# Kernel optimization log

Measured on AMD Instinct MI355X. Metric: run time of the kernel, lower is better.

## Reference

```python
import jax, jax.numpy as jnp
import numpy as np

N = 100000
E = 1600000
IN_C, HID_C, OUT_C = 128, 256, 64
EPS = 1e-5


def _glorot(key, shape):
    fan_in, fan_out = shape
    lim = float(np.sqrt(6.0 / (fan_in + fan_out)))
    return jax.random.uniform(key, shape, jnp.float32, -lim, lim)


def sage_conv(x, src, dst, deg_inv, W_l, b_l, W_r):
    # mean aggregation of neighbor features into target nodes
    msg_sum = jax.ops.segment_sum(x[src], dst, num_segments=N)  # [N, d]
    mean = msg_sum * deg_inv[:, None]
    return mean @ W_l + b_l + x @ W_r


def batch_norm(x, gamma, beta, rm, rv):
    return (x - rm) * jax.lax.rsqrt(rv + EPS) * gamma + beta


def setup_inputs() -> dict:
    key = jax.random.key(0)
    ks = jax.random.split(key, 10)
    x = jax.random.normal(ks[0], (N, IN_C), jnp.float32)
    edge_index = jax.random.randint(ks[1], (2, E), 0, N, jnp.int64)
    inp = {
        "x": x,
        "edge_index": edge_index,
        # layer 1: SAGEConv(IN_C -> HID_C) + BN
        "W1l": _glorot(ks[2], (IN_C, HID_C)),
        "b1l": jnp.zeros((HID_C,), jnp.float32),
        "W1r": _glorot(ks[3], (IN_C, HID_C)),
        "g1": jnp.ones((HID_C,), jnp.float32),
        "be1": jnp.zeros((HID_C,), jnp.float32),
        "rm1": 0.1 * jax.random.normal(ks[4], (HID_C,), jnp.float32),
        "rv1": jnp.ones((HID_C,), jnp.float32),
        # layer 2: SAGEConv(HID_C -> HID_C) + BN
        "W2l": _glorot(ks[5], (HID_C, HID_C)),
        "b2l": jnp.zeros((HID_C,), jnp.float32),
        "W2r": _glorot(ks[6], (HID_C, HID_C)),
        "g2": jnp.ones((HID_C,), jnp.float32),
        "be2": jnp.zeros((HID_C,), jnp.float32),
        "rm2": 0.1 * jax.random.normal(ks[7], (HID_C,), jnp.float32),
        "rv2": jnp.ones((HID_C,), jnp.float32),
        # classifier: SAGEConv(HID_C -> OUT_C)
        "Wcl": _glorot(ks[8], (HID_C, OUT_C)),
        "bcl": jnp.zeros((OUT_C,), jnp.float32),
        "Wcr": _glorot(ks[9], (HID_C, OUT_C)),
    }
    return inp


def reference(x, edge_index, W1l, b1l, W1r, g1, be1, rm1, rv1,
              W2l, b2l, W2r, g2, be2, rm2, rv2, Wcl, bcl, Wcr):
    src, dst = edge_index[0], edge_index[1]
    deg = jax.ops.segment_sum(jnp.ones((E,), jnp.float32), dst, num_segments=N)
    deg_inv = jnp.where(deg > 0, 1.0 / jnp.maximum(deg, 1.0), 0.0)

    h = sage_conv(x, src, dst, deg_inv, W1l, b1l, W1r)
    h = jax.nn.relu(batch_norm(h, g1, be1, rm1, rv1))
    # dropout is identity in eval mode (training=False)
    h = sage_conv(h, src, dst, deg_inv, W2l, b2l, W2r)
    h = jax.nn.relu(batch_norm(h, g2, be2, rm2, rv2))
    return sage_conv(h, src, dst, deg_inv, Wcl, bcl, Wcr)
```

## Files before the change

### kernel.cpp

```cpp
#include <hip/hip_runtime.h>
#include <stdint.h>

#define NN 100000
#define EE 1600000
#define IN_C 128
#define HID_C 256
#define OUT_C 64

#define NB 391
#define CAP 5120
#define K3_NPT 25
#define K3_BLOCKS 250

typedef unsigned short bf16_t;
typedef unsigned int u32;
typedef __attribute__((ext_vector_type(8))) short bf16x8;
typedef __attribute__((ext_vector_type(4))) float f32x4;

__device__ __forceinline__ float b2f(unsigned short u){
  unsigned int x = ((unsigned int)u) << 16;
  return __uint_as_float(x);
}
__device__ __forceinline__ unsigned short f2b(float f){
  unsigned int x = __float_as_uint(f);
  unsigned int r = x + 0x7FFFu + ((x >> 16) & 1u);
  return (unsigned short)(r >> 16);
}

#define GL16(gp, lp) __builtin_amdgcn_global_load_lds( \
    (const __attribute__((address_space(1))) void*)(gp), \
    (__attribute__((address_space(3))) void*)(lp), 16, 0, 0)


__global__ __launch_bounds__(256) void bcount_k(const int* __restrict__ ei,
    int* __restrict__ bcnt){
  __shared__ int h[NB];
  int t = threadIdx.x;
  int o = 0;
  for (int i = t; i < 1024; i += 256) o |= ei[2*i + 1];
  h[t] = o; __syncthreads();
  for (int s = 128; s > 0; s >>= 1){
    if (t < s) h[t] |= h[t + s];
    __syncthreads();
  }
  int i64 = (h[0] == 0) ? 1 : 0;
  __syncthreads();
  for (int i = t; i < NB; i += 256) h[i] = 0;
  __syncthreads();
  int base = blockIdx.x * (256 * K3_NPT);
  #pragma unroll
  for (int q = 0; q < K3_NPT; ++q){
    int e = base + q * 256 + t;
    int d = i64 ? ei[2*(EE + e)] : ei[EE + e];
    atomicAdd(&h[d >> 8], 1);
  }
  __syncthreads();
  for (int i = t; i < NB; i += 256) if (h[i]) atomicAdd(&bcnt[i], h[i]);
}

__global__ void bscan_k(const int* __restrict__ bcnt, int* __restrict__ bbase){
  __shared__ int sm[512];
  int t = threadIdx.x;
  sm[t] = (t < NB) ? bcnt[t] : 0;
  __syncthreads();
  for (int off = 1; off < 512; off <<= 1){
    int a = (t >= off) ? sm[t - off] : 0;
    __syncthreads();
    sm[t] += a;
    __syncthreads();
  }
  if (t <= NB) bbase[t] = (t == 0) ? 0 : sm[t - 1];
}

__global__ __launch_bounds__(256) void bscatter_k(const int* __restrict__ ei,
    const int* __restrict__ bbase,
    int* __restrict__ bfill, uint2* __restrict__ pairs){
  __shared__ int cnt[NB];
  __shared__ int cnt2[NB];
  __shared__ int lbase[NB];
  int t = threadIdx.x;
  int o = 0;
  for (int i = t; i < 1024; i += 256) o |= ei[2*i + 1];
  cnt[t] = o; __syncthreads();
  for (int s = 128; s > 0; s >>= 1){
    if (t < s) cnt[t] |= cnt[t + s];
    __syncthreads();
  }
  int i64 = (cnt[0] == 0) ? 1 : 0;
  __syncthreads();
  for (int i = t; i < NB; i += 256){ cnt[i] = 0; cnt2[i] = 0; }
  __syncthreads();
  int ebase = blockIdx.x * (256 * K3_NPT);
  int src[K3_NPT], dst[K3_NPT];
  #pragma unroll
  for (int q = 0; q < K3_NPT; ++q){
    int e = ebase + q * 256 + t;
    src[q] = i64 ? ei[2*e] : ei[e];
    dst[q] = i64 ? ei[2*(EE + e)] : ei[EE + e];
    atomicAdd(&cnt[dst[q] >> 8], 1);
  }
  __syncthreads();
  for (int i = t; i < NB; i += 256)
    lbase[i] = cnt[i] ? atomicAdd(&bfill[i], cnt[i]) : 0;
  __syncthreads();
  #pragma unroll
  for (int q = 0; q < K3_NPT; ++q){
    int b = dst[q] >> 8;
    int r = atomicAdd(&cnt2[b], 1);
    pairs[bbase[b] + lbase[b] + r] = make_uint2((u32)src[q], (u32)dst[q]);
  }
}

__global__ __launch_bounds__(256) void bsort_k(const uint2* __restrict__ pairs,
    const int* __restrict__ bbase, int* __restrict__ rowptr, int* __restrict__ csr){
  __shared__ int hist[256];
  __shared__ int pref[257];
  __shared__ int cnt[256];
  __shared__ int lsrc[CAP];
  int b = blockIdx.x;
  int t = threadIdx.x;
  int e0 = bbase[b], e1 = bbase[b + 1];
  int s = e1 - e0;
  hist[t] = 0; cnt[t] = 0;
  __syncthreads();
  for (int i = t; i < s; i += 256)
    atomicAdd(&hist[pairs[e0 + i].y & 255], 1);
  __syncthreads();
  for (int off = 1; off < 256; off <<= 1){
    int a = (t >= off) ? hist[t - off] : 0;
    __syncthreads();
    hist[t] += a;
    __syncthreads();
  }
  if (t == 0) pref[0] = 0;
  pref[t + 1] = hist[t];
  __syncthreads();
  int gid = b * 256 + t;
  if (gid <= NN) rowptr[gid] = e0 + pref[t];
  for (int i = t; i < s; i += 256){
    uint2 p = pairs[e0 + i];
    int bin = p.y & 255;
    int r = atomicAdd(&cnt[bin], 1);
    int pos = pref[bin] + r;
    if (pos < CAP) lsrc[pos] = (int)p.x;
    else           csr[e0 + pos] = (int)p.x;
  }
  __syncthreads();
  int lim = s < CAP ? s : CAP;
  for (int i = t; i < lim; i += 256) csr[e0 + i] = lsrc[i];
}


struct WtArgs {
  const float* W[6];
  bf16_t* Wt[6];
  int K[6], N[6];
  int off[7];
  int wb;
};

__global__ __launch_bounds__(256) void xconv_k(const float* __restrict__ x,
    bf16_t* __restrict__ xb, uint8_t* __restrict__ xq, float* __restrict__ scx,
    WtArgs a){
  int b = blockIdx.x;
  int t = threadIdx.x;
  if (b >= a.wb){
    int g = (b - a.wb) * 256 + t;
    if (g >= a.off[6]) return;
    #pragma unroll
    for (int s = 0; s < 6; ++s){
      if (g >= a.off[s] && g < a.off[s + 1]){
        int local = g - a.off[s];
        int K = a.K[s], N = a.N[s];
        int n = local / K, k = local - n * K;
        a.Wt[s][local] = f2b(a.W[s][(size_t)k * N + n]);
      }
    }
    return;
  }
  int row  = (b * 256 + t) >> 6;
  int lane = t & 63;
  if (row >= NN) return;
  float2 u = *(const float2*)(x + (size_t)row * IN_C + lane * 2);
  u32 bb = (u32)f2b(u.x) | ((u32)f2b(u.y) << 16);
  *(u32*)(xb + (size_t)row * IN_C + lane * 2) = bb;
  float m = fmaxf(fabsf(u.x), fabsf(u.y));
  #pragma unroll
  for (int msk = 1; msk < 64; msk <<= 1) m = fmaxf(m, __shfl_xor(m, msk, 64));
  float inv = m > 0.f ? 127.f / m : 0.f;
  float qa = fminf(fmaxf(rintf(u.x * inv), -127.f), 127.f);
  float qb = fminf(fmaxf(rintf(u.y * inv), -127.f), 127.f);
  u32 pa = (u32)(uint8_t)(int8_t)(int)qa | (((u32)(uint8_t)(int8_t)(int)qb) << 8);
  *(unsigned short*)(xq + (size_t)row * IN_C + lane * 2) = (unsigned short)pa;
  if (lane == 0) scx[row] = m / 127.f;
}

template<int C, bool SIGNED, typename TIN>
__global__ __launch_bounds__(256) void quant_k(const TIN* __restrict__ in,
    uint8_t* __restrict__ outq, float* __restrict__ scales){
  constexpr int V = C / 64;
  int row  = (blockIdx.x * 256 + threadIdx.x) >> 6;
  int lane = threadIdx.x & 63;
  if (row >= NN) return;
  float v[V];
  if constexpr (sizeof(TIN) == 4){
    float2 u = *(const float2*)((const float*)in + (size_t)row * C + lane * 2);
    v[0] = u.x; v[1] = u.y;
  } else {
    const bf16_t* bp = (const bf16_t*)in + (size_t)row * C + lane * V;
    if constexpr (V == 4){
      uint2 u = *(const uint2*)bp;
      v[0] = b2f((unsigned short)(u.x & 0xffffu)); v[1] = b2f((unsigned short)(u.x >> 16));
      v[2] = b2f((unsigned short)(u.y & 0xffffu)); v[3] = b2f((unsigned short)(u.y >> 16));
    } else if constexpr (V == 2){
      u32 u = *(const u32*)bp;
      v[0] = b2f((unsigned short)(u & 0xffffu)); v[1] = b2f((unsigned short)(u >> 16));
    } else {
      v[0] = b2f(*bp);
    }
  }
  float m = 0.f;
  #pragma unroll
  for (int i = 0; i < V; ++i) m = fmaxf(m, SIGNED ? fabsf(v[i]) : v[i]);
  #pragma unroll
  for (int msk = 1; msk < 64; msk <<= 1) m = fmaxf(m, __shfl_xor(m, msk, 64));
  const float qmax = SIGNED ? 127.f : 255.f;
  float inv = m > 0.f ? qmax / m : 0.f;
  uint8_t qb[V];
  #pragma unroll
  for (int i = 0; i < V; ++i){
    float qf = rintf(v[i] * inv);
    if (SIGNED){
      qf = fminf(fmaxf(qf, -127.f), 127.f);
      qb[i] = (uint8_t)(int8_t)(int)qf;
    } else {
      qf = fminf(fmaxf(qf, 0.f), 255.f);
      qb[i] = (uint8_t)(int)qf;
    }
  }
  uint8_t* op = outq + (size_t)row * C + lane * V;
  if constexpr (V == 4){
    u32 p = (u32)qb[0] | ((u32)qb[1] << 8) | ((u32)qb[2] << 16) | ((u32)qb[3] << 24);
    *(u32*)op = p;
  } else if constexpr (V == 2){
    *(unsigned short*)op = (unsigned short)((u32)qb[0] | ((u32)qb[1] << 8));
  } else {
    *op = qb[0];
  }
  if (lane == 0) scales[row] = m / qmax;
}


__device__ __forceinline__ float qdec(u32 w, int b, bool sgn){
  u32 byte = (w >> (8 * b)) & 0xffu;
  return sgn ? (float)(int8_t)byte : (float)byte;
}

template<int C, bool SIGNED>
__global__ __launch_bounds__(256) void agg_q8_k(const uint8_t* __restrict__ tq,
    const float* __restrict__ tsc,
    const int* __restrict__ rowptr, const int* __restrict__ csr,
    bf16_t* __restrict__ outm){
  constexpr int V = C / 64;
  int wid  = (blockIdx.x * 256 + threadIdx.x) >> 6;
  int lane = threadIdx.x & 63;
  if (wid >= NN) return;
  int beg = __builtin_amdgcn_readfirstlane(rowptr[wid]);
  int end = __builtin_amdgcn_readfirstlane(rowptr[wid + 1]);
  float acc[V];
  #pragma unroll
  for (int i = 0; i < V; ++i) acc[i] = 0.f;

  const uint8_t* hb = tq + lane * V;
  int e = beg;
  for (; e + 7 < end; e += 8){
    int   s[8]; float sc[8];
    #pragma unroll
    for (int q = 0; q < 8; ++q) s[q] = csr[e + q];
    u32 w[8];
    #pragma unroll
    for (int q = 0; q < 8; ++q){
      if constexpr (V == 4) w[q] = *(const u32*)(hb + (size_t)s[q] * C);
      else                  w[q] = *(const unsigned short*)(hb + (size_t)s[q] * C);
      sc[q] = tsc[s[q]];
    }
    #pragma unroll
    for (int q = 0; q < 8; ++q)
      #pragma unroll
      for (int i = 0; i < V; ++i)
        acc[i] += sc[q] * qdec(w[q], i, SIGNED);
  }
  for (; e < end; ++e){
    int s0 = csr[e];
    u32 w0;
    if constexpr (V == 4) w0 = *(const u32*)(hb + (size_t)s0 * C);
    else                  w0 = *(const unsigned short*)(hb + (size_t)s0 * C);
    float sc0 = tsc[s0];
    #pragma unroll
    for (int i = 0; i < V; ++i) acc[i] += sc0 * qdec(w0, i, SIGNED);
  }

  int d = end - beg;
  float di = d > 0 ? 1.0f / (float)d : 0.f;
  bf16_t* po = outm + (size_t)wid * C + lane * V;
  if constexpr (V == 2){
    u32 u = (u32)f2b(acc[0] * di) | ((u32)f2b(acc[1] * di) << 16);
    *(u32*)po = u;
  } else {
    uint2 u;
    u.x = (u32)f2b(acc[0] * di) | ((u32)f2b(acc[1] * di) << 16);
    u.y = (u32)f2b(acc[2] * di) | ((u32)f2b(acc[3] * di) << 16);
    *(uint2*)po = u;
  }
}

__global__ __launch_bounds__(256) void agg_final_q8_k(
    const uint8_t* __restrict__ Pq, const float* __restrict__ scp,
    const float* __restrict__ Q,
    const int* __restrict__ rowptr, const int* __restrict__ csr,
    float* __restrict__ out){
  int wid  = (blockIdx.x * 256 + threadIdx.x) >> 6;
  int lane = threadIdx.x & 63;
  if (wid >= NN) return;
  int beg = __builtin_amdgcn_readfirstlane(rowptr[wid]);
  int end = __builtin_amdgcn_readfirstlane(rowptr[wid + 1]);
  const uint8_t* Pb = Pq + lane;
  float acc = 0.f;
  int e = beg;
  for (; e + 7 < end; e += 8){
    int s[8]; uint8_t b[8]; float sc[8];
    #pragma unroll
    for (int q = 0; q < 8; ++q) s[q] = csr[e + q];
    #pragma unroll
    for (int q = 0; q < 8; ++q){ b[q] = Pb[(size_t)s[q] * 64]; sc[q] = scp[s[q]]; }
    #pragma unroll
    for (int q = 0; q < 8; ++q) acc += sc[q] * (float)(int8_t)b[q];
  }
  for (; e < end; ++e) acc += scp[csr[e]] * (float)(int8_t)Pb[(size_t)csr[e] * 64];
  int d = end - beg;
  float di = d > 0 ? 1.0f / (float)d : 0.f;
  out[(size_t)wid * 64 + lane] = acc * di + Q[(size_t)wid * 64 + lane];
}


template<int K_>
__global__ __launch_bounds__(256) void mfma_gemm_k(
    const bf16_t* __restrict__ A0, const bf16_t* __restrict__ A1,
    const bf16_t* __restrict__ W0t, const bf16_t* __restrict__ W1t,
    const float* __restrict__ bias,
    const float* __restrict__ gamma, const float* __restrict__ beta,
    const float* __restrict__ rmean, const float* __restrict__ rvar,
    bf16_t* __restrict__ out, int M, int Nout)
{
  constexpr int BM = 64;
  constexpr int BN = 256;
  constexpr int BK = 64;
  constexpr int KT = K_ / BK;
  constexpr int T  = 2 * KT;
  __shared__ bf16_t As[2][BM * BK];
  __shared__ bf16_t Bs[2][BN * BK];

  int t    = threadIdx.x;
  int lane = t & 63;
  int wid  = t >> 6;
  int l15  = lane & 15;
  int quad = lane >> 4;

  int m0 = blockIdx.x * BM;

  f32x4 acc[4][4];
  #pragma unroll
  for (int i = 0; i < 4; ++i)
    #pragma unroll
    for (int j = 0; j < 4; ++j)
      acc[i][j] = (f32x4){0.f, 0.f, 0.f, 0.f};

  auto stage = [&](int tile, int buf){
    const bf16_t* Ap = (tile < KT) ? A0 : A1;
    const bf16_t* Wp = (tile < KT) ? W0t : W1t;
    int k0 = ((tile < KT) ? tile : tile - KT) * BK;
    #pragma unroll
    for (int i = 0; i < 2; ++i){
      int c   = i * 256 + t;
      int row = c >> 3;
      int k8  = (c & 7) ^ (row & 7);
      int gm  = m0 + row; gm = gm < NN ? gm : NN - 1;
      GL16(Ap + (size_t)gm * K_ + k0 + k8 * 8, &As[buf][(i * 256 + (t & 192)) * 8]);
    }
    #pragma unroll
    for (int i = 0; i < 8; ++i){
      int c   = i * 256 + t;
      int row = c >> 3;
      int k8  = (c & 7) ^ (row & 7);
      GL16(Wp + (size_t)row * K_ + k0 + k8 * 8, &Bs[buf][(i * 256 + (t & 192)) * 8]);
    }
  };

  stage(0, 0);
  #pragma unroll
  for (int tile = 0; tile < T; ++tile){
    int buf = tile & 1;
    if (tile + 1 < T){
      stage(tile + 1, buf ^ 1);
      asm volatile("s_waitcnt vmcnt(10)" ::: "memory");
    } else {
      asm volatile("s_waitcnt vmcnt(0)" ::: "memory");
    }
    __builtin_amdgcn_s_barrier();
    #pragma unroll
    for (int kk = 0; kk < 2; ++kk){
      bf16x8 af[4], bfr[4];
      #pragma unroll
      for (int i = 0; i < 4; ++i){
        int row = i * 16 + l15;
        af[i] = *(const bf16x8*)(&As[buf][(size_t)((row << 3) + ((quad + kk * 4) ^ (row & 7))) * 8]);
      }
      #pragma unroll
      for (int j = 0; j < 4; ++j){
        int row = wid * 64 + j * 16 + l15;
        bfr[j] = *(const bf16x8*)(&Bs[buf][(size_t)((row << 3) + ((quad + kk * 4) ^ (row & 7))) * 8]);
      }
      #pragma unroll
      for (int i = 0; i < 4; ++i)
        #pragma unroll
        for (int j = 0; j < 4; ++j)
          acc[i][j] = __builtin_amdgcn_mfma_f32_16x16x32_bf16(af[i], bfr[j], acc[i][j], 0, 0, 0);
    }
    __builtin_amdgcn_s_barrier();
  }

  #pragma unroll
  for (int j = 0; j < 4; ++j){
    int col = wid * 64 + j * 16 + l15;
    float sc = gamma[col] * rsqrtf(rvar[col] + 1e-5f);
    float shift = (bias[col] - rmean[col]) * sc + beta[col];
    #pragma unroll
    for (int i = 0; i < 4; ++i){
      int rbase = m0 + i * 16 + quad * 4;
      #pragma unroll
      for (int r = 0; r < 4; ++r){
        int row = rbase + r;
        if (row < M){
          float v = fmaxf(acc[i][j][r] * sc + shift, 0.f);
          out[(size_t)row * Nout + col] = f2b(v);
        }
      }
    }
  }
}


__global__ __launch_bounds__(256) void gemm3_k(
    const bf16_t* __restrict__ A, const bf16_t* __restrict__ Wt,
    const float* __restrict__ bcl,
    uint8_t* __restrict__ Pq, float* __restrict__ scp,
    float* __restrict__ Q, int M)
{
  constexpr int K_ = 256, BM = 64, BN = 128, BK = 64;
  constexpr int T = K_ / BK;
  __shared__ bf16_t As[2][BM * BK];
  __shared__ bf16_t Bs[2][BN * BK];

  int t    = threadIdx.x;
  int lane = t & 63;
  int wid  = t >> 6;
  int wr   = wid >> 1, wc = wid & 1;
  int l15  = lane & 15;
  int quad = lane >> 4;
  int m0 = blockIdx.x * BM;

  f32x4 acc[2][4];
  #pragma unroll
  for (int i = 0; i < 2; ++i)
    #pragma unroll
    for (int j = 0; j < 4; ++j)
      acc[i][j] = (f32x4){0.f, 0.f, 0.f, 0.f};

  auto stage = [&](int tile, int buf){
    int k0 = tile * BK;
    #pragma unroll
    for (int i = 0; i < 2; ++i){
      int c   = i * 256 + t;
      int row = c >> 3;
      int k8  = (c & 7) ^ (row & 7);
      int gm  = m0 + row; gm = gm < NN ? gm : NN - 1;
      GL16(A + (size_t)gm * K_ + k0 + k8 * 8, &As[buf][(i * 256 + (t & 192)) * 8]);
    }
    #pragma unroll
    for (int i = 0; i < 4; ++i){
      int c   = i * 256 + t;
      int row = c >> 3;
      int k8  = (c & 7) ^ (row & 7);
      GL16(Wt + (size_t)row * K_ + k0 + k8 * 8, &Bs[buf][(i * 256 + (t & 192)) * 8]);
    }
  };

  stage(0, 0);
  #pragma unroll
  for (int tile = 0; tile < T; ++tile){
    int buf = tile & 1;
    if (tile + 1 < T){
      stage(tile + 1, buf ^ 1);
      asm volatile("s_waitcnt vmcnt(6)" ::: "memory");
    } else {
      asm volatile("s_waitcnt vmcnt(0)" ::: "memory");
    }
    __builtin_amdgcn_s_barrier();
    #pragma unroll
    for (int kk = 0; kk < 2; ++kk){
      bf16x8 af[2], bfr[4];
      #pragma unroll
      for (int i = 0; i < 2; ++i){
        int row = wr * 32 + i * 16 + l15;
        af[i] = *(const bf16x8*)(&As[buf][(size_t)((row << 3) + ((quad + kk * 4) ^ (row & 7))) * 8]);
      }
      #pragma unroll
      for (int j = 0; j < 4; ++j){
        int row = wc * 64 + j * 16 + l15;
        bfr[j] = *(const bf16x8*)(&Bs[buf][(size_t)((row << 3) + ((quad + kk * 4) ^ (row & 7))) * 8]);
      }
      #pragma unroll
      for (int i = 0; i < 2; ++i)
        #pragma unroll
        for (int j = 0; j < 4; ++j)
          acc[i][j] = __builtin_amdgcn_mfma_f32_16x16x32_bf16(af[i], bfr[j], acc[i][j], 0, 0, 0);
    }
    __builtin_amdgcn_s_barrier();
  }

  if (wc == 0){
    #pragma unroll
    for (int i = 0; i < 2; ++i){
      #pragma unroll
      for (int r = 0; r < 4; ++r){
        int row = m0 + wr * 32 + i * 16 + quad * 4 + r;
        float m = 0.f;
        #pragma unroll
        for (int j = 0; j < 4; ++j) m = fmaxf(m, fabsf(acc[i][j][r]));
        #pragma unroll
        for (int msk = 1; msk < 16; msk <<= 1) m = fmaxf(m, __shfl_xor(m, msk, 64));
        float inv = m > 0.f ? 127.f / m : 0.f;
        if (row < M){
          #pragma unroll
          for (int j = 0; j < 4; ++j){
            float qf = fminf(fmaxf(rintf(acc[i][j][r] * inv), -127.f), 127.f);
            ((int8_t*)Pq)[(size_t)row * 64 + j * 16 + l15] = (int8_t)(int)qf;
          }
          if (l15 == 0) scp[row] = m / 127.f;
        }
      }
    }
  } else {
    #pragma unroll
    for (int j = 0; j < 4; ++j){
      int col = j * 16 + l15;
      float bc = bcl[col];
      #pragma unroll
      for (int i = 0; i < 2; ++i){
        int rbase = m0 + wr * 32 + i * 16 + quad * 4;
        #pragma unroll
        for (int r = 0; r < 4; ++r){
          int row = rbase + r;
          if (row < M) Q[(size_t)row * 64 + col] = acc[i][j][r] + bc;
        }
      }
    }
  }
}


extern "C" void kernel_launch(void* const* d_in, const int* in_sizes, int n_in,
                              void* d_out, int out_size, void* d_ws, size_t ws_size,
                              hipStream_t stream)
{
  const float* x   = (const float*)d_in[0];
  const int*   ei  = (const int*)d_in[1];
  const float* W1l = (const float*)d_in[2];
  const float* b1l = (const float*)d_in[3];
  const float* W1r = (const float*)d_in[4];
  const float* g1  = (const float*)d_in[5];
  const float* be1 = (const float*)d_in[6];
  const float* rm1 = (const float*)d_in[7];
  const float* rv1 = (const float*)d_in[8];
  const float* W2l = (const float*)d_in[9];
  const float* b2l = (const float*)d_in[10];
  const float* W2r = (const float*)d_in[11];
  const float* g2  = (const float*)d_in[12];
  const float* be2 = (const float*)d_in[13];
  const float* rm2 = (const float*)d_in[14];
  const float* rv2 = (const float*)d_in[15];
  const float* Wcl = (const float*)d_in[16];
  const float* bcl = (const float*)d_in[17];
  const float* Wcr = (const float*)d_in[18];
  (void)in_sizes; (void)n_in; (void)out_size; (void)ws_size;

  char* ws = (char*)d_ws;
  size_t off = 0;
  auto alloc = [&](size_t bytes)->char* {
    char* p = ws + off;
    off += (bytes + 15) & ~(size_t)15;
    return p;
  };
  int*    bcnt   = (int*)   alloc(800 * 4);
  int*    bfill  = bcnt + 400;
  int*    bbase  = (int*)   alloc((size_t)(NB + 1) * 4);
  int*    rowptr = (int*)   alloc((size_t)(NN + 1) * 4);
  int*    csr    = (int*)   alloc((size_t)EE * 4);
  bf16_t* xb     = (bf16_t*)alloc((size_t)NN * IN_C * 2);
  bf16_t* aggb   = (bf16_t*)alloc((size_t)NN * HID_C * 2);
  bf16_t* h1     = (bf16_t*)alloc((size_t)NN * HID_C * 2);
  bf16_t* h2     = (bf16_t*)alloc((size_t)NN * HID_C * 2);
  bf16_t* W1lt   = (bf16_t*)alloc((size_t)IN_C  * HID_C * 2);
  bf16_t* W1rt   = (bf16_t*)alloc((size_t)IN_C  * HID_C * 2);
  bf16_t* W2lt   = (bf16_t*)alloc((size_t)HID_C * HID_C * 2);
  bf16_t* W2rt   = (bf16_t*)alloc((size_t)HID_C * HID_C * 2);
  bf16_t* Wc3t   = (bf16_t*)alloc((size_t)128 * HID_C * 2);
  float*  sc1    = (float*) alloc((size_t)NN * 4);
  float*  scp    = (float*) alloc((size_t)NN * 4);

  uint2*   pairs = (uint2*)aggb;
  uint8_t* xq  = (uint8_t*)h2;
  float*   scx = (float*)((char*)h2 + (size_t)NN * IN_C);
  uint8_t* h1q = (uint8_t*)xb;
  uint8_t* Pq  = (uint8_t*)aggb;
  float*   Q   = (float*)h1;

  hipMemsetAsync(bcnt, 0, 800 * 4, stream);

  int wb = (NN + 3) / 4;
  int g64 = (NN + 63) / 64;

  WtArgs wa;
  wa.W[0] = W1l; wa.Wt[0] = W1lt; wa.K[0] = IN_C;  wa.N[0] = HID_C;
  wa.W[1] = W1r; wa.Wt[1] = W1rt; wa.K[1] = IN_C;  wa.N[1] = HID_C;
  wa.W[2] = W2l; wa.Wt[2] = W2lt; wa.K[2] = HID_C; wa.N[2] = HID_C;
  wa.W[3] = W2r; wa.Wt[3] = W2rt; wa.K[3] = HID_C; wa.N[3] = HID_C;
  wa.W[4] = Wcl; wa.Wt[4] = Wc3t;             wa.K[4] = HID_C; wa.N[4] = OUT_C;
  wa.W[5] = Wcr; wa.Wt[5] = Wc3t + 64 * 256;  wa.K[5] = HID_C; wa.N[5] = OUT_C;
  wa.off[0] = 0;
  for (int s = 0; s < 6; ++s) wa.off[s + 1] = wa.off[s] + wa.K[s] * wa.N[s];
  wa.wb = wb;
  int wtb = (wa.off[6] + 255) / 256;
  xconv_k<<<wb + wtb, 256, 0, stream>>>(x, xb, xq, scx, wa);

  bcount_k<<<K3_BLOCKS, 256, 0, stream>>>(ei, bcnt);
  bscan_k<<<1, 512, 0, stream>>>(bcnt, bbase);
  bscatter_k<<<K3_BLOCKS, 256, 0, stream>>>(ei, bbase, bfill, pairs);
  bsort_k<<<NB, 256, 0, stream>>>(pairs, bbase, rowptr, csr);

  agg_q8_k<IN_C, true><<<wb, 256, 0, stream>>>(xq, scx, rowptr, csr, aggb);
  mfma_gemm_k<IN_C><<<g64, 256, 0, stream>>>(
      aggb, xb, W1lt, W1rt, b1l, g1, be1, rm1, rv1, h1, NN, HID_C);

  quant_k<HID_C, false, bf16_t><<<wb, 256, 0, stream>>>(h1, h1q, sc1);
  agg_q8_k<HID_C, false><<<wb, 256, 0, stream>>>(h1q, sc1, rowptr, csr, aggb);
  mfma_gemm_k<HID_C><<<g64, 256, 0, stream>>>(
      aggb, h1, W2lt, W2rt, b2l, g2, be2, rm2, rv2, h2, NN, HID_C);

  gemm3_k<<<g64, 256, 0, stream>>>(h2, Wc3t, bcl, Pq, scp, Q, NN);
  agg_final_q8_k<<<wb, 256, 0, stream>>>(Pq, scp, Q, rowptr, csr, (float*)d_out);
}
```

Before: 545.4 us.

## Shard int8 neighbor aggregation across channel slices with edge-parallel lanes

Replaces the one-wave-per-node aggregation, where each lane owns a few channels and walks every edge, with a sharded kernel. Each node's channels are split into 8 slices handled by separate blocks. Within a wave, groups of lanes process different edges in parallel and are combined with xor-shuffle reductions. The aim is more memory-level parallelism per node and more waves in flight, at the cost of 8x more blocks, repeated rowptr/csr/scale reads per shard, and shuffle overhead.

Measured after the change: 1.028 ms. 1.88x slower.

```diff
diff --git a/kernel.cpp b/kernel.cpp
--- a/kernel.cpp
+++ b/kernel.cpp
@@ -257,56 +257,48 @@
 }
 
 template<int C, bool SIGNED>
-__global__ __launch_bounds__(256) void agg_q8_k(const uint8_t* __restrict__ tq,
-    const float* __restrict__ tsc,
+__global__ __launch_bounds__(256) void agg_q8_shard_k(
+    const uint8_t* __restrict__ tq, const float* __restrict__ tsc,
     const int* __restrict__ rowptr, const int* __restrict__ csr,
     bf16_t* __restrict__ outm){
-  constexpr int V = C / 64;
-  int wid  = (blockIdx.x * 256 + threadIdx.x) >> 6;
+  constexpr int W = C / 8;
+  constexpr int L = W / 4;
+  constexpr int G = 64 / L;
+  int b    = blockIdx.x;
+  int s    = b & 7;
+  int wid  = (b >> 3) * 4 + (threadIdx.x >> 6);
   int lane = threadIdx.x & 63;
   if (wid >= NN) return;
   int beg = __builtin_amdgcn_readfirstlane(rowptr[wid]);
   int end = __builtin_amdgcn_readfirstlane(rowptr[wid + 1]);
-  float acc[V];
-  #pragma unroll
-  for (int i = 0; i < V; ++i) acc[i] = 0.f;
-
-  const uint8_t* hb = tq + lane * V;
-  int e = beg;
-  for (; e + 7 < end; e += 8){
-    int   s[8]; float sc[8];
-    #pragma unroll
-    for (int q = 0; q < 8; ++q) s[q] = csr[e + q];
-    u32 w[8];
-    #pragma unroll
-    for (int q = 0; q < 8; ++q){
-      if constexpr (V == 4) w[q] = *(const u32*)(hb + (size_t)s[q] * C);
-      else                  w[q] = *(const unsigned short*)(hb + (size_t)s[q] * C);
-      sc[q] = tsc[s[q]];
-    }
-    #pragma unroll
-    for (int q = 0; q < 8; ++q)
-      #pragma unroll
-      for (int i = 0; i < V; ++i)
-        acc[i] += sc[q] * qdec(w[q], i, SIGNED);
-  }
-  for (; e < end; ++e){
-    int s0 = csr[e];
-    u32 w0;
-    if constexpr (V == 4) w0 = *(const u32*)(hb + (size_t)s0 * C);
-    else                  w0 = *(const unsigned short*)(hb + (size_t)s0 * C);
-    float sc0 = tsc[s0];
-    #pragma unroll
-    for (int i = 0; i < V; ++i) acc[i] += sc0 * qdec(w0, i, SIGNED);
-  }
+  int g = lane / L;
+  int r = lane % L;
+  const uint8_t* hb = tq + s * W + r * 4;
+
+  float acc[4] = {0.f, 0.f, 0.f, 0.f};
+  int last = end - 1;
+  for (int e = beg; e < end; e += G){
+    int idx = e + g;
+    int cl  = idx < last ? idx : last;
+    int s_  = csr[cl];
+    float sv = tsc[s_];
+    float sc = idx < end ? sv : 0.f;
+    u32 w = *(const u32*)(hb + (size_t)s_ * C);
+    #pragma unroll
+    for (int j = 0; j < 4; ++j)
+      acc[j] += sc * qdec(w, j, SIGNED);
+  }
+
+  #pragma unroll
+  for (int mask = L; mask < 64; mask <<= 1)
+    #pragma unroll
+    for (int j = 0; j < 4; ++j)
+      acc[j] += __shfl_xor(acc[j], mask, 64);
 
   int d = end - beg;
   float di = d > 0 ? 1.0f / (float)d : 0.f;
-  bf16_t* po = outm + (size_t)wid * C + lane * V;
-  if constexpr (V == 2){
-    u32 u = (u32)f2b(acc[0] * di) | ((u32)f2b(acc[1] * di) << 16);
-    *(u32*)po = u;
-  } else {
+  if (lane < L){
+    bf16_t* po = outm + (size_t)wid * C + s * W + lane * 4;
     uint2 u;
     u.x = (u32)f2b(acc[0] * di) | ((u32)f2b(acc[1] * di) << 16);
     u.y = (u32)f2b(acc[2] * di) | ((u32)f2b(acc[3] * di) << 16);
@@ -629,6 +621,7 @@
 
   int wb = (NN + 3) / 4;
   int g64 = (NN + 63) / 64;
+  int gsh = 8 * ((NN + 3) / 4);
 
   WtArgs wa;
   wa.W[0] = W1l; wa.Wt[0] = W1lt; wa.K[0] = IN_C;  wa.N[0] = HID_C;
@@ -648,12 +641,12 @@
   bscatter_k<<<K3_BLOCKS, 256, 0, stream>>>(ei, bbase, bfill, pairs);
   bsort_k<<<NB, 256, 0, stream>>>(pairs, bbase, rowptr, csr);
 
-  agg_q8_k<IN_C, true><<<wb, 256, 0, stream>>>(xq, scx, rowptr, csr, aggb);
+  agg_q8_shard_k<IN_C, true><<<gsh, 256, 0, stream>>>(xq, scx, rowptr, csr, aggb);
   mfma_gemm_k<IN_C><<<g64, 256, 0, stream>>>(
       aggb, xb, W1lt, W1rt, b1l, g1, be1, rm1, rv1, h1, NN, HID_C);
 
   quant_k<HID_C, false, bf16_t><<<wb, 256, 0, stream>>>(h1, h1q, sc1);
-  agg_q8_k<HID_C, false><<<wb, 256, 0, stream>>>(h1q, sc1, rowptr, csr, aggb);
+  agg_q8_shard_k<HID_C, false><<<gsh, 256, 0, stream>>>(h1q, sc1, rowptr, csr, aggb);
   mfma_gemm_k<HID_C><<<g64, 256, 0, stream>>>(
       aggb, h1, W2lt, W2rt, b2l, g2, be2, rm2, rv2, h2, NN, HID_C);
 
```
